# Optimization experiments

Measured on AMD Instinct MI355X. Metric: run time of the kernel, lower is better.

The kernel has to match this reference:

```python
import jax, jax.numpy as jnp
import numpy as np

N_NODES = 131072
N_EDGES = 2097152
N_GRAPHS = 2048
IN_CH, HID, OUT = 12, 64, 4


def gcn_conv(x, W, b, src, dst, n_nodes):
    """PyG GCNConv: out = D^{-1/2} (A + I) D^{-1/2} (x W) + b.
    Degree computed at target nodes including self loops (edge_weight=1)."""
    h = x @ W  # [N, F_out]
    # degree with self loops: in-degree + 1
    deg = jax.ops.segment_sum(jnp.ones((src.shape[0],), x.dtype), dst,
                              num_segments=n_nodes) + 1.0
    dinv = jax.lax.rsqrt(deg)  # [N]
    norm = dinv[src] * dinv[dst]  # [E]
    # scatter-add messages from src to dst
    agg = jax.ops.segment_sum(h[src] * norm[:, None], dst, num_segments=n_nodes)
    # self-loop contribution: norm_ii = dinv[i]^2
    agg = agg + h * (dinv * dinv)[:, None]
    return agg + b


def global_mean_pool(x, batch, n_graphs):
    sums = jax.ops.segment_sum(x, batch, num_segments=n_graphs)
    cnt = jax.ops.segment_sum(jnp.ones((x.shape[0],), x.dtype), batch,
                              num_segments=n_graphs)
    return sums / jnp.maximum(cnt, 1.0)[:, None]


def setup_inputs() -> dict:
    key = jax.random.key(0)
    ks = jax.random.split(key, 9)
    x = jax.random.normal(ks[0], (N_NODES, IN_CH), dtype=jnp.float32)
    edge_index = jax.random.randint(ks[1], (2, N_EDGES), 0, N_NODES, dtype=jnp.int64)
    batch = jnp.sort(jax.random.randint(ks[2], (N_NODES,), 0, N_GRAPHS, dtype=jnp.int64))
    def glorot(k, shape):
        lim = np.sqrt(6.0 / (shape[0] + shape[1]))
        return jax.random.uniform(k, shape, jnp.float32, -lim, lim)
    return {
        "x": x,
        "edge_index": edge_index,
        "batch": batch,
        "W1": glorot(ks[3], (IN_CH, HID)),
        "b1": jnp.zeros((HID,), jnp.float32),
        "W2": glorot(ks[4], (HID, HID)),
        "b2": jnp.zeros((HID,), jnp.float32),
        "Wfc": glorot(ks[5], (HID, OUT)),
        "bfc": jnp.zeros((OUT,), jnp.float32),
    }


def reference(x, edge_index, batch, W1, b1, W2, b2, Wfc, bfc):
    src, dst = edge_index[0], edge_index[1]
    h = jax.nn.relu(gcn_conv(x, W1, b1, src, dst, N_NODES))
    h = jax.nn.relu(gcn_conv(h, W2, b2, src, dst, N_NODES))
    g = global_mean_pool(h, batch, N_GRAPHS)  # [n_graphs, HID]
    return jax.nn.sigmoid(g @ Wfc + bfc)  # [n_graphs, OUT]
```

## Files before the change

### kernel.cpp

```cpp
#include <hip/hip_runtime.h>
#include <hip/hip_bf16.h>


#define N_NODES 131072
#define N_EDGES 2097152
#define N_GRAPHS 2048
#define IN_CH 12
#define HID 64
#define OUT_CH 4
#define NBUCK 512
#define CHUNK 8192
#define STRIDE 4608
#define CSR_STRIDE 5120
#define CAP 5120

typedef float f32x2 __attribute__((ext_vector_type(2)));

__device__ __forceinline__ unsigned short f2bf(float f) {
    unsigned u = __float_as_uint(f);
    return (unsigned short)((u + 0x7fffu + ((u >> 16) & 1u)) >> 16);
}
__device__ __forceinline__ unsigned pack2bf(float lo, float hi) {
    return (unsigned)f2bf(lo) | ((unsigned)f2bf(hi) << 16);
}
__device__ __forceinline__ float bflo(unsigned v) { return __uint_as_float(v << 16); }
__device__ __forceinline__ float bfhi(unsigned v) { return __uint_as_float(v & 0xFFFF0000u); }

__global__ __launch_bounds__(1024, 4)
void bucket_kernel(const int* __restrict__ src, const int* __restrict__ dst,
                   int* __restrict__ bucket_count, int* __restrict__ staged) {
    __shared__ int hist[NBUCK];
    __shared__ int lscan[NBUCK];
    __shared__ int gbase[NBUCK];
    __shared__ int cursor[NBUCK];
    __shared__ int sorted[CHUNK];
    int tid = threadIdx.x;
    int base = blockIdx.x * CHUNK;
    if (tid < NBUCK) { hist[tid] = 0; cursor[tid] = 0; }
    __syncthreads();
    int d8[8], s8[8];
#pragma unroll
    for (int k = 0; k < 8; k++) {
        int i = base + k * 1024 + tid;
        d8[k] = dst[i];
        s8[k] = src[i];
        atomicAdd(&hist[d8[k] >> 8], 1);
    }
    __syncthreads();
    if (tid < NBUCK) lscan[tid] = hist[tid];
    __syncthreads();
    for (int off = 1; off < NBUCK; off <<= 1) {
        int u = (tid < NBUCK && tid >= off) ? lscan[tid - off] : 0;
        __syncthreads();
        if (tid < NBUCK) lscan[tid] += u;
        __syncthreads();
    }
    if (tid < NBUCK) gbase[tid] = atomicAdd(&bucket_count[tid], hist[tid]);
    __syncthreads();
#pragma unroll
    for (int k = 0; k < 8; k++) {
        int b = d8[k] >> 8;
        int start = lscan[b] - hist[b];
        int p = start + atomicAdd(&cursor[b], 1);
        sorted[p] = ((d8[k] & 255) << 17) | s8[k];
    }
    __syncthreads();
    int wid = tid >> 6, lane = tid & 63;
    int g16 = lane >> 4, k16 = lane & 15;
    for (int b0 = wid * 4; b0 < NBUCK; b0 += 64) {
        int b = b0 + g16;
        int cb = hist[b];
        int lbase = lscan[b] - cb;
        int gb = b * STRIDE + gbase[b];
        for (int k = k16; k < cb; k += 16) staged[gb + k] = sorted[lbase + k];
    }
}

__global__ void build_kernel(const int* __restrict__ bucket_count, const int* __restrict__ staged,
                             int2* __restrict__ rowbounds, float* __restrict__ dinv,
                             int* __restrict__ csr, const float* __restrict__ x,
                             unsigned short* __restrict__ xb) {
    __shared__ int sl[STRIDE];
    __shared__ int image[CAP];
    __shared__ int cnt[256];
    __shared__ int scn[256];
    __shared__ int loff[256];
    __shared__ int cursor[256];
    __shared__ int totalS;
    int b = blockIdx.x;
    int tid = threadIdx.x;
    int count = bucket_count[b];
    const int* st = staged + b * STRIDE;
    cnt[tid] = 0;
    cursor[tid] = 0;
    for (int i = tid; i < count; i += 256) sl[i] = st[i];
    __syncthreads();
    for (int i = tid; i < count; i += 256) atomicAdd(&cnt[(sl[i] >> 17) & 255], 1);
    __syncthreads();
    int deg = cnt[tid];
    int degp = (deg + 3) & ~3;
    scn[tid] = degp;
    __syncthreads();
    for (int off = 1; off < 256; off <<= 1) {
        int u = (tid >= off) ? scn[tid - off] : 0;
        __syncthreads();
        scn[tid] += u;
        __syncthreads();
    }
    int lo = scn[tid] - degp;
    loff[tid] = lo;
    int nbase = (b << 8) + tid;
    int gb = b * CSR_STRIDE;
    rowbounds[nbase] = make_int2(gb + lo, gb + lo + degp);
    float dv = rsqrtf((float)deg + 1.0f);
    dinv[nbase] = dv;
    if (tid == 255) totalS = lo + degp;
    {
        const float* xp = x + nbase * IN_CH;
        unsigned o[8];
#pragma unroll
        for (int k = 0; k < 6; k++) o[k] = pack2bf(dv * xp[2 * k], dv * xp[2 * k + 1]);
        o[6] = 0; o[7] = 0;
        uint4* dstp = (uint4*)(xb + nbase * 16);
        dstp[0] = make_uint4(o[0], o[1], o[2], o[3]);
        dstp[1] = make_uint4(o[4], o[5], o[6], o[7]);
    }
    if (b == 0 && tid < 2)
        ((uint4*)(xb + (size_t)N_NODES * 16))[tid] = make_uint4(0, 0, 0, 0);
    __syncthreads();
    for (int i = tid; i < count; i += 256) {
        int rec = sl[i];
        int s = rec & 0x1FFFF;
        int dq = (rec >> 17) & 255;
        int p = loff[dq] + atomicAdd(&cursor[dq], 1);
        int val = s << 6;
        if (p < CAP) image[p] = val;
        else csr[gb + p] = val;
    }
    __syncthreads();
    int padval = N_NODES << 6;
    for (int p = loff[tid] + deg; p < loff[tid] + degp; p++) {
        if (p < CAP) image[p] = padval;
        else csr[gb + p] = padval;
    }
    __syncthreads();
    int lim = totalS < CAP ? totalS : CAP;
    int* dstp = csr + gb;
    for (int i = tid; i < lim; i += 256) dstp[i] = image[i];
}

__global__ __launch_bounds__(256, 6)
void w1w2_kernel(const int2* __restrict__ rowbounds, const int* __restrict__ csr,
                 const float* __restrict__ dinv, const unsigned short* __restrict__ xb,
                 const float* __restrict__ W1, const float* __restrict__ b1,
                 const float* __restrict__ W2, unsigned int* __restrict__ hout) {
    __shared__ float sW1[IN_CH * HID];
    __shared__ float sA[64 * 17];
    __shared__ float sh1t[HID * 65];
    int tid = threadIdx.x;
    for (int i = tid; i < IN_CH * HID; i += 256) sW1[i] = W1[i];
    int node0 = blockIdx.x * 64;
    {
        int nl = tid >> 2;
        int node = node0 + nl;
        int p = tid & 1, qoff = 8 * p;
        int2 rb = rowbounds[node];
        float dn = dinv[node];
        uint4 su = make_uint4(0, 0, 0, 0);
        if (!(tid & 2)) su = *(const uint4*)(xb + node * 16 + qoff);
        int len = rb.y - rb.x;
        int hlen = (len >> 3) << 2;
        int beg = (tid & 2) ? rb.x + hlen : rb.x;
        int end = (tid & 2) ? rb.y : rb.x + hlen;
        f32x2 a0[4] = {{0, 0}, {0, 0}, {0, 0}, {0, 0}};
        f32x2 a1[4] = {{0, 0}, {0, 0}, {0, 0}, {0, 0}};
        f32x2 a2[4] = {{0, 0}, {0, 0}, {0, 0}, {0, 0}};
        f32x2 a3[4] = {{0, 0}, {0, 0}, {0, 0}, {0, 0}};
        for (int j = beg; j < end; j += 4) {
            int4 e = *(const int4*)(csr + j);
            uint4 u0 = *(const uint4*)(xb + (e.x >> 2) + qoff);
            uint4 u1 = *(const uint4*)(xb + (e.y >> 2) + qoff);
            uint4 u2 = *(const uint4*)(xb + (e.z >> 2) + qoff);
            uint4 u3 = *(const uint4*)(xb + (e.w >> 2) + qoff);
            a0[0] += (f32x2){bflo(u0.x), bfhi(u0.x)};
            a0[1] += (f32x2){bflo(u0.y), bfhi(u0.y)};
            a0[2] += (f32x2){bflo(u0.z), bfhi(u0.z)};
            a0[3] += (f32x2){bflo(u0.w), bfhi(u0.w)};
            a1[0] += (f32x2){bflo(u1.x), bfhi(u1.x)};
            a1[1] += (f32x2){bflo(u1.y), bfhi(u1.y)};
            a1[2] += (f32x2){bflo(u1.z), bfhi(u1.z)};
            a1[3] += (f32x2){bflo(u1.w), bfhi(u1.w)};
            a2[0] += (f32x2){bflo(u2.x), bfhi(u2.x)};
            a2[1] += (f32x2){bflo(u2.y), bfhi(u2.y)};
            a2[2] += (f32x2){bflo(u2.z), bfhi(u2.z)};
            a2[3] += (f32x2){bflo(u2.w), bfhi(u2.w)};
            a3[0] += (f32x2){bflo(u3.x), bfhi(u3.x)};
            a3[1] += (f32x2){bflo(u3.y), bfhi(u3.y)};
            a3[2] += (f32x2){bflo(u3.z), bfhi(u3.z)};
            a3[3] += (f32x2){bflo(u3.w), bfhi(u3.w)};
        }
        f32x2 s0 = (a0[0] + a1[0]) + (a2[0] + a3[0]);
        f32x2 s1 = (a0[1] + a1[1]) + (a2[1] + a3[1]);
        f32x2 s2 = (a0[2] + a1[2]) + (a2[2] + a3[2]);
        f32x2 s3 = (a0[3] + a1[3]) + (a2[3] + a3[3]);
        s0[0] += __shfl_xor(s0[0], 2); s0[1] += __shfl_xor(s0[1], 2);
        s1[0] += __shfl_xor(s1[0], 2); s1[1] += __shfl_xor(s1[1], 2);
        s2[0] += __shfl_xor(s2[0], 2); s2[1] += __shfl_xor(s2[1], 2);
        s3[0] += __shfl_xor(s3[0], 2); s3[1] += __shfl_xor(s3[1], 2);
        if (!(tid & 2)) {
            s0 += (f32x2){bflo(su.x), bfhi(su.x)};
            s1 += (f32x2){bflo(su.y), bfhi(su.y)};
            s2 += (f32x2){bflo(su.z), bfhi(su.z)};
            s3 += (f32x2){bflo(su.w), bfhi(su.w)};
            float* dp = &sA[nl * 17 + qoff];
            dp[0] = dn * s0[0]; dp[1] = dn * s0[1];
            dp[2] = dn * s1[0]; dp[3] = dn * s1[1];
            dp[4] = dn * s2[0]; dp[5] = dn * s2[1];
            dp[6] = dn * s3[0]; dp[7] = dn * s3[1];
        }
    }
    __syncthreads();
    int w = tid >> 6, c = tid & 63;
    float bc = b1[c];
#pragma unroll
    for (int it = 0; it < 4; it++) {
        int n0 = w * 16 + it * 4;
        float a0 = bc, a1 = bc, a2 = bc, a3 = bc;
#pragma unroll
        for (int k = 0; k < IN_CH; k++) {
            float wv = sW1[k * HID + c];
            a0 += sA[(n0 + 0) * 17 + k] * wv;
            a1 += sA[(n0 + 1) * 17 + k] * wv;
            a2 += sA[(n0 + 2) * 17 + k] * wv;
            a3 += sA[(n0 + 3) * 17 + k] * wv;
        }
        float4 o = make_float4(fmaxf(a0, 0.0f), fmaxf(a1, 0.0f),
                               fmaxf(a2, 0.0f), fmaxf(a3, 0.0f));
        *(float4*)&sh1t[c * 65 + n0] = o;
    }
    __syncthreads();
    int nq = tid >> 4, c4 = (tid & 15) * 4;
    float4 a0 = {0, 0, 0, 0}, a1 = {0, 0, 0, 0}, a2 = {0, 0, 0, 0}, a3 = {0, 0, 0, 0};
#pragma unroll 4
    for (int k = 0; k < HID; k++) {
        float4 wv = *(const float4*)&W2[k * HID + c4];
        float4 hv = *(const float4*)&sh1t[k * 65 + nq * 4];
        a0.x += hv.x * wv.x; a0.y += hv.x * wv.y; a0.z += hv.x * wv.z; a0.w += hv.x * wv.w;
        a1.x += hv.y * wv.x; a1.y += hv.y * wv.y; a1.z += hv.y * wv.z; a1.w += hv.y * wv.w;
        a2.x += hv.z * wv.x; a2.y += hv.z * wv.y; a2.z += hv.z * wv.z; a2.w += hv.z * wv.w;
        a3.x += hv.w * wv.x; a3.y += hv.w * wv.y; a3.z += hv.w * wv.z; a3.w += hv.w * wv.w;
    }
    int nb = node0 + nq * 4;
    float dv0 = dinv[nb + 0], dv1 = dinv[nb + 1], dv2 = dinv[nb + 2], dv3 = dinv[nb + 3];
    unsigned int p0 = (unsigned int)__builtin_amdgcn_cvt_pk_fp8_f32(dv0 * a0.x, dv0 * a0.y, 0, false);
    p0 = (unsigned int)__builtin_amdgcn_cvt_pk_fp8_f32(dv0 * a0.z, dv0 * a0.w, (int)p0, true);
    unsigned int p1 = (unsigned int)__builtin_amdgcn_cvt_pk_fp8_f32(dv1 * a1.x, dv1 * a1.y, 0, false);
    p1 = (unsigned int)__builtin_amdgcn_cvt_pk_fp8_f32(dv1 * a1.z, dv1 * a1.w, (int)p1, true);
    unsigned int p2 = (unsigned int)__builtin_amdgcn_cvt_pk_fp8_f32(dv2 * a2.x, dv2 * a2.y, 0, false);
    p2 = (unsigned int)__builtin_amdgcn_cvt_pk_fp8_f32(dv2 * a2.z, dv2 * a2.w, (int)p2, true);
    unsigned int p3 = (unsigned int)__builtin_amdgcn_cvt_pk_fp8_f32(dv3 * a3.x, dv3 * a3.y, 0, false);
    p3 = (unsigned int)__builtin_amdgcn_cvt_pk_fp8_f32(dv3 * a3.z, dv3 * a3.w, (int)p3, true);
    int cl = c4 >> 2;
    hout[(nb + 0) * 16 + cl] = p0;
    hout[(nb + 1) * 16 + cl] = p1;
    hout[(nb + 2) * 16 + cl] = p2;
    hout[(nb + 3) * 16 + cl] = p3;
    if (blockIdx.x == 0 && tid < 16)
        hout[(size_t)N_NODES * 16 + tid] = 0;
}

__device__ __forceinline__ void add_fp8q(f32x2* a, uint4 u) {
    a[0] += __builtin_amdgcn_cvt_pk_f32_fp8((int)u.x, false);
    a[1] += __builtin_amdgcn_cvt_pk_f32_fp8((int)u.x, true);
    a[2] += __builtin_amdgcn_cvt_pk_f32_fp8((int)u.y, false);
    a[3] += __builtin_amdgcn_cvt_pk_f32_fp8((int)u.y, true);
    a[4] += __builtin_amdgcn_cvt_pk_f32_fp8((int)u.z, false);
    a[5] += __builtin_amdgcn_cvt_pk_f32_fp8((int)u.z, true);
    a[6] += __builtin_amdgcn_cvt_pk_f32_fp8((int)u.w, false);
    a[7] += __builtin_amdgcn_cvt_pk_f32_fp8((int)u.w, true);
}

__device__ __forceinline__ void agg_body16(int beg, int end, const int* __restrict__ csr,
                                           const unsigned char* __restrict__ h,
                                           int qoff, float* r) {
    f32x2 a0[8] = {{0, 0}, {0, 0}, {0, 0}, {0, 0}, {0, 0}, {0, 0}, {0, 0}, {0, 0}};
    f32x2 a1[8] = {{0, 0}, {0, 0}, {0, 0}, {0, 0}, {0, 0}, {0, 0}, {0, 0}, {0, 0}};
    int j = beg;
    for (; j + 8 <= end; j += 8) {
        int4 ea = *(const int4*)(csr + j);
        int4 eb = *(const int4*)(csr + j + 4);
        uint4 u0 = *(const uint4*)(h + ea.x + qoff);
        uint4 u1 = *(const uint4*)(h + ea.y + qoff);
        uint4 u2 = *(const uint4*)(h + ea.z + qoff);
        uint4 u3 = *(const uint4*)(h + ea.w + qoff);
        uint4 u4 = *(const uint4*)(h + eb.x + qoff);
        uint4 u5 = *(const uint4*)(h + eb.y + qoff);
        uint4 u6 = *(const uint4*)(h + eb.z + qoff);
        uint4 u7 = *(const uint4*)(h + eb.w + qoff);
        add_fp8q(a0, u0); add_fp8q(a1, u1); add_fp8q(a0, u2); add_fp8q(a1, u3);
        add_fp8q(a0, u4); add_fp8q(a1, u5); add_fp8q(a0, u6); add_fp8q(a1, u7);
    }
    if (j < end) {
        int4 ea = *(const int4*)(csr + j);
        uint4 u0 = *(const uint4*)(h + ea.x + qoff);
        uint4 u1 = *(const uint4*)(h + ea.y + qoff);
        uint4 u2 = *(const uint4*)(h + ea.z + qoff);
        uint4 u3 = *(const uint4*)(h + ea.w + qoff);
        add_fp8q(a0, u0); add_fp8q(a1, u1); add_fp8q(a0, u2); add_fp8q(a1, u3);
    }
#pragma unroll
    for (int k = 0; k < 8; k++) {
        f32x2 s = a0[k] + a1[k];
        r[2 * k] = s[0];
        r[2 * k + 1] = s[1];
    }
}

__global__ void agg_pool_kernel(const int2* __restrict__ rowbounds, const int* __restrict__ csr,
                                const float* __restrict__ dinv,
                                const unsigned char* __restrict__ h,
                                const float* __restrict__ b, const int* __restrict__ batch,
                                float* __restrict__ pool, float* __restrict__ gcnt) {
    __shared__ float red[64][HID + 4];
    __shared__ int gids[64];
    int tid = threadIdx.x;
    int w = tid >> 6, lane = tid & 63, sub = lane >> 2, q = lane & 3;
    int qoff = 16 * q;
    int node = (blockIdx.x * 4 + w) * 16 + sub;
    int2 rb = rowbounds[node];
    float dn = dinv[node];
    float r[16];
    agg_body16(rb.x, rb.y, csr, h, qoff, r);
    uint4 su = *(const uint4*)(h + node * HID + qoff);
    f32x2 s[8];
    s[0] = __builtin_amdgcn_cvt_pk_f32_fp8((int)su.x, false);
    s[1] = __builtin_amdgcn_cvt_pk_f32_fp8((int)su.x, true);
    s[2] = __builtin_amdgcn_cvt_pk_f32_fp8((int)su.y, false);
    s[3] = __builtin_amdgcn_cvt_pk_f32_fp8((int)su.y, true);
    s[4] = __builtin_amdgcn_cvt_pk_f32_fp8((int)su.z, false);
    s[5] = __builtin_amdgcn_cvt_pk_f32_fp8((int)su.z, true);
    s[6] = __builtin_amdgcn_cvt_pk_f32_fp8((int)su.w, false);
    s[7] = __builtin_amdgcn_cvt_pk_f32_fp8((int)su.w, true);
    int nl = w * 16 + sub;
    float* rp = &red[nl][qoff];
#pragma unroll
    for (int k = 0; k < 4; k++) {
        float4 bv = *(const float4*)&b[qoff + 4 * k];
        rp[4 * k + 0] = fmaxf(dn * (r[4 * k + 0] + s[2 * k][0]) + bv.x, 0.0f);
        rp[4 * k + 1] = fmaxf(dn * (r[4 * k + 1] + s[2 * k][1]) + bv.y, 0.0f);
        rp[4 * k + 2] = fmaxf(dn * (r[4 * k + 2] + s[2 * k + 1][0]) + bv.z, 0.0f);
        rp[4 * k + 3] = fmaxf(dn * (r[4 * k + 3] + s[2 * k + 1][1]) + bv.w, 0.0f);
    }
    if (q == 0) gids[nl] = batch[node];
    __syncthreads();
    if (tid < 64) {
        int c = tid;
        float acc = 0.0f;
        int cur = gids[0], cnt = 0;
        for (int n = 0; n < 64; n++) {
            int g = gids[n];
            if (g != cur) {
                atomicAdd(&pool[cur * HID + c], acc);
                if (c == 0) atomicAdd(&gcnt[cur], (float)cnt);
                acc = 0.0f; cnt = 0; cur = g;
            }
            acc += red[n][c];
            cnt++;
        }
        atomicAdd(&pool[cur * HID + c], acc);
        if (c == 0) atomicAdd(&gcnt[cur], (float)cnt);
    }
}

__global__ void final_kernel(const float* __restrict__ pool, const float* __restrict__ gcnt,
                             const float* __restrict__ Wfc, const float* __restrict__ bfc,
                             float* __restrict__ out) {
    int idx = blockIdx.x * 256 + threadIdx.x;
    if (idx >= N_GRAPHS * OUT_CH) return;
    int g = idx >> 2, o = idx & 3;
    float inv = 1.0f / fmaxf(gcnt[g], 1.0f);
    float acc = bfc[o];
#pragma unroll
    for (int k = 0; k < HID; k++) acc += pool[g * HID + k] * inv * Wfc[k * OUT_CH + o];
    out[idx] = 1.0f / (1.0f + expf(-acc));
}

extern "C" void kernel_launch(void* const* d_in, const int* in_sizes, int n_in,
                              void* d_out, int out_size, void* d_ws, size_t ws_size,
                              hipStream_t stream) {
    const float* x   = (const float*)d_in[0];
    const int* eidx  = (const int*)d_in[1];
    const int* batch = (const int*)d_in[2];
    const float* W1  = (const float*)d_in[3];
    const float* b1  = (const float*)d_in[4];
    const float* W2  = (const float*)d_in[5];
    const float* b2  = (const float*)d_in[6];
    const float* Wfc = (const float*)d_in[7];
    const float* bfc = (const float*)d_in[8];
    float* out = (float*)d_out;

    const int* src = eidx;
    const int* dst = eidx + N_EDGES;

    unsigned char* hB = (unsigned char*)d_ws;
    int*   csr    = (int*)(hB + (size_t)(N_NODES + 1) * HID);
    int*   staged = csr + (size_t)NBUCK * CSR_STRIDE;
    float* dinv   = (float*)(staged + (size_t)NBUCK * STRIDE);
    int2*  rowbounds = (int2*)(dinv + N_NODES);
    int*   bucket_count = (int*)(rowbounds + N_NODES);
    float* pool   = (float*)(bucket_count + NBUCK);
    float* gcnt   = pool + N_GRAPHS * HID;
    unsigned short* xb = (unsigned short*)(gcnt + N_GRAPHS);

    hipMemsetAsync(bucket_count, 0,
                   (size_t)(NBUCK + N_GRAPHS * HID + N_GRAPHS) * 4, stream);

    bucket_kernel<<<N_EDGES / CHUNK, 1024, 0, stream>>>(src, dst, bucket_count, staged);
    build_kernel<<<NBUCK, 256, 0, stream>>>(bucket_count, staged, rowbounds, dinv, csr, x, xb);

    w1w2_kernel<<<N_NODES / 64, 256, 0, stream>>>(rowbounds, csr, dinv, xb, W1, b1, W2,
                                                  (unsigned int*)hB);

    agg_pool_kernel<<<N_NODES / 64, 256, 0, stream>>>(rowbounds, csr, dinv, hB, b2, batch,
                                                      pool, gcnt);

    final_kernel<<<(N_GRAPHS * OUT_CH + 255) / 256, 256, 0, stream>>>(pool, gcnt, Wfc, bfc, out);
}
```

Baseline: 180.8 us.

## Pack bf16 node features to 24-byte rows and unroll first-layer gather

Stores the scaled bf16 input features as 12 values (24 bytes) per node instead of a padded 32-byte row, so each gathered neighbor row in the first-layer aggregation moves less data. The gather loop is unrolled to eight edges per iteration with a remainder step, W1 is held in registers instead of shared memory, and the launch bound is raised to allow more resident blocks. In the pooling kernel, the self-feature and batch-id loads are hoisted ahead of the neighbor aggregation to overlap their latency. Risks include unaligned 12-byte loads and a changed index decode (3*(e>>4)) that must match the CSR encoding of s<<6.

Result: no change. 182.3 us (+0.8%).

```diff
diff --git a/kernel.cpp b/kernel.cpp
--- a/kernel.cpp
+++ b/kernel.cpp
@@ -117,16 +117,16 @@
     if (tid == 255) totalS = lo + degp;
     {
         const float* xp = x + nbase * IN_CH;
-        unsigned o[8];
+        unsigned o[6];
 #pragma unroll
         for (int k = 0; k < 6; k++) o[k] = pack2bf(dv * xp[2 * k], dv * xp[2 * k + 1]);
-        o[6] = 0; o[7] = 0;
-        uint4* dstp = (uint4*)(xb + nbase * 16);
-        dstp[0] = make_uint4(o[0], o[1], o[2], o[3]);
-        dstp[1] = make_uint4(o[4], o[5], o[6], o[7]);
-    }
-    if (b == 0 && tid < 2)
-        ((uint4*)(xb + (size_t)N_NODES * 16))[tid] = make_uint4(0, 0, 0, 0);
+        uint2* dstp = (uint2*)(xb + nbase * 12);
+        dstp[0] = make_uint2(o[0], o[1]);
+        dstp[1] = make_uint2(o[2], o[3]);
+        dstp[2] = make_uint2(o[4], o[5]);
+    }
+    if (b == 0 && tid < 3)
+        ((uint2*)(xb + (size_t)N_NODES * 12))[tid] = make_uint2(0, 0);
     __syncthreads();
     for (int i = tid; i < count; i += 256) {
         int rec = sl[i];
@@ -149,90 +149,93 @@
     for (int i = tid; i < lim; i += 256) dstp[i] = image[i];
 }
 
-__global__ __launch_bounds__(256, 6)
+__device__ __forceinline__ void acc3(f32x2* a, uint3 u) {
+    a[0] += (f32x2){bflo(u.x), bfhi(u.x)};
+    a[1] += (f32x2){bflo(u.y), bfhi(u.y)};
+    a[2] += (f32x2){bflo(u.z), bfhi(u.z)};
+}
+
+__global__ __launch_bounds__(256, 8)
 void w1w2_kernel(const int2* __restrict__ rowbounds, const int* __restrict__ csr,
                  const float* __restrict__ dinv, const unsigned short* __restrict__ xb,
                  const float* __restrict__ W1, const float* __restrict__ b1,
                  const float* __restrict__ W2, unsigned int* __restrict__ hout) {
-    __shared__ float sW1[IN_CH * HID];
-    __shared__ float sA[64 * 17];
+    __shared__ float sA[64 * 13];
     __shared__ float sh1t[HID * 65];
     int tid = threadIdx.x;
-    for (int i = tid; i < IN_CH * HID; i += 256) sW1[i] = W1[i];
     int node0 = blockIdx.x * 64;
     {
         int nl = tid >> 2;
         int node = node0 + nl;
-        int p = tid & 1, qoff = 8 * p;
+        int p = tid & 1, soff = 6 * p;
         int2 rb = rowbounds[node];
         float dn = dinv[node];
-        uint4 su = make_uint4(0, 0, 0, 0);
-        if (!(tid & 2)) su = *(const uint4*)(xb + node * 16 + qoff);
+        uint3 su = {0, 0, 0};
+        if (!(tid & 2)) su = *(const uint3*)(xb + node * 12 + soff);
         int len = rb.y - rb.x;
         int hlen = (len >> 3) << 2;
         int beg = (tid & 2) ? rb.x + hlen : rb.x;
         int end = (tid & 2) ? rb.y : rb.x + hlen;
-        f32x2 a0[4] = {{0, 0}, {0, 0}, {0, 0}, {0, 0}};
-        f32x2 a1[4] = {{0, 0}, {0, 0}, {0, 0}, {0, 0}};
-        f32x2 a2[4] = {{0, 0}, {0, 0}, {0, 0}, {0, 0}};
-        f32x2 a3[4] = {{0, 0}, {0, 0}, {0, 0}, {0, 0}};
-        for (int j = beg; j < end; j += 4) {
-            int4 e = *(const int4*)(csr + j);
-            uint4 u0 = *(const uint4*)(xb + (e.x >> 2) + qoff);
-            uint4 u1 = *(const uint4*)(xb + (e.y >> 2) + qoff);
-            uint4 u2 = *(const uint4*)(xb + (e.z >> 2) + qoff);
-            uint4 u3 = *(const uint4*)(xb + (e.w >> 2) + qoff);
-            a0[0] += (f32x2){bflo(u0.x), bfhi(u0.x)};
-            a0[1] += (f32x2){bflo(u0.y), bfhi(u0.y)};
-            a0[2] += (f32x2){bflo(u0.z), bfhi(u0.z)};
-            a0[3] += (f32x2){bflo(u0.w), bfhi(u0.w)};
-            a1[0] += (f32x2){bflo(u1.x), bfhi(u1.x)};
-            a1[1] += (f32x2){bflo(u1.y), bfhi(u1.y)};
-            a1[2] += (f32x2){bflo(u1.z), bfhi(u1.z)};
-            a1[3] += (f32x2){bflo(u1.w), bfhi(u1.w)};
-            a2[0] += (f32x2){bflo(u2.x), bfhi(u2.x)};
-            a2[1] += (f32x2){bflo(u2.y), bfhi(u2.y)};
-            a2[2] += (f32x2){bflo(u2.z), bfhi(u2.z)};
-            a2[3] += (f32x2){bflo(u2.w), bfhi(u2.w)};
-            a3[0] += (f32x2){bflo(u3.x), bfhi(u3.x)};
-            a3[1] += (f32x2){bflo(u3.y), bfhi(u3.y)};
-            a3[2] += (f32x2){bflo(u3.z), bfhi(u3.z)};
-            a3[3] += (f32x2){bflo(u3.w), bfhi(u3.w)};
+        f32x2 a0[3] = {{0, 0}, {0, 0}, {0, 0}};
+        f32x2 a1[3] = {{0, 0}, {0, 0}, {0, 0}};
+        f32x2 a2[3] = {{0, 0}, {0, 0}, {0, 0}};
+        f32x2 a3[3] = {{0, 0}, {0, 0}, {0, 0}};
+        int j = beg;
+        for (; j + 8 <= end; j += 8) {
+            int4 ea = *(const int4*)(csr + j);
+            int4 eb = *(const int4*)(csr + j + 4);
+            uint3 u0 = *(const uint3*)(xb + 3 * (ea.x >> 4) + soff);
+            uint3 u1 = *(const uint3*)(xb + 3 * (ea.y >> 4) + soff);
+            uint3 u2 = *(const uint3*)(xb + 3 * (ea.z >> 4) + soff);
+            uint3 u3 = *(const uint3*)(xb + 3 * (ea.w >> 4) + soff);
+            uint3 u4 = *(const uint3*)(xb + 3 * (eb.x >> 4) + soff);
+            uint3 u5 = *(const uint3*)(xb + 3 * (eb.y >> 4) + soff);
+            uint3 u6 = *(const uint3*)(xb + 3 * (eb.z >> 4) + soff);
+            uint3 u7 = *(const uint3*)(xb + 3 * (eb.w >> 4) + soff);
+            acc3(a0, u0); acc3(a1, u1); acc3(a2, u2); acc3(a3, u3);
+            acc3(a0, u4); acc3(a1, u5); acc3(a2, u6); acc3(a3, u7);
+        }
+        if (j < end) {
+            int4 ea = *(const int4*)(csr + j);
+            uint3 u0 = *(const uint3*)(xb + 3 * (ea.x >> 4) + soff);
+            uint3 u1 = *(const uint3*)(xb + 3 * (ea.y >> 4) + soff);
+            uint3 u2 = *(const uint3*)(xb + 3 * (ea.z >> 4) + soff);
+            uint3 u3 = *(const uint3*)(xb + 3 * (ea.w >> 4) + soff);
+            acc3(a0, u0); acc3(a1, u1); acc3(a2, u2); acc3(a3, u3);
         }
         f32x2 s0 = (a0[0] + a1[0]) + (a2[0] + a3[0]);
         f32x2 s1 = (a0[1] + a1[1]) + (a2[1] + a3[1]);
         f32x2 s2 = (a0[2] + a1[2]) + (a2[2] + a3[2]);
-        f32x2 s3 = (a0[3] + a1[3]) + (a2[3] + a3[3]);
         s0[0] += __shfl_xor(s0[0], 2); s0[1] += __shfl_xor(s0[1], 2);
         s1[0] += __shfl_xor(s1[0], 2); s1[1] += __shfl_xor(s1[1], 2);
         s2[0] += __shfl_xor(s2[0], 2); s2[1] += __shfl_xor(s2[1], 2);
-        s3[0] += __shfl_xor(s3[0], 2); s3[1] += __shfl_xor(s3[1], 2);
         if (!(tid & 2)) {
             s0 += (f32x2){bflo(su.x), bfhi(su.x)};
             s1 += (f32x2){bflo(su.y), bfhi(su.y)};
             s2 += (f32x2){bflo(su.z), bfhi(su.z)};
-            s3 += (f32x2){bflo(su.w), bfhi(su.w)};
-            float* dp = &sA[nl * 17 + qoff];
+            float* dp = &sA[nl * 13 + soff];
             dp[0] = dn * s0[0]; dp[1] = dn * s0[1];
             dp[2] = dn * s1[0]; dp[3] = dn * s1[1];
             dp[4] = dn * s2[0]; dp[5] = dn * s2[1];
-            dp[6] = dn * s3[0]; dp[7] = dn * s3[1];
         }
     }
     __syncthreads();
     int w = tid >> 6, c = tid & 63;
     float bc = b1[c];
+    float wk[IN_CH];
+#pragma unroll
+    for (int k = 0; k < IN_CH; k++) wk[k] = W1[k * HID + c];
 #pragma unroll
     for (int it = 0; it < 4; it++) {
         int n0 = w * 16 + it * 4;
         float a0 = bc, a1 = bc, a2 = bc, a3 = bc;
 #pragma unroll
         for (int k = 0; k < IN_CH; k++) {
-            float wv = sW1[k * HID + c];
-            a0 += sA[(n0 + 0) * 17 + k] * wv;
-            a1 += sA[(n0 + 1) * 17 + k] * wv;
-            a2 += sA[(n0 + 2) * 17 + k] * wv;
-            a3 += sA[(n0 + 3) * 17 + k] * wv;
+            float wv = wk[k];
+            a0 += sA[(n0 + 0) * 13 + k] * wv;
+            a1 += sA[(n0 + 1) * 13 + k] * wv;
+            a2 += sA[(n0 + 2) * 13 + k] * wv;
+            a3 += sA[(n0 + 3) * 13 + k] * wv;
         }
         float4 o = make_float4(fmaxf(a0, 0.0f), fmaxf(a1, 0.0f),
                                fmaxf(a2, 0.0f), fmaxf(a3, 0.0f));
@@ -329,9 +332,10 @@
     int node = (blockIdx.x * 4 + w) * 16 + sub;
     int2 rb = rowbounds[node];
     float dn = dinv[node];
+    uint4 su = *(const uint4*)(h + node * HID + qoff);
+    int gid = batch[node];
     float r[16];
     agg_body16(rb.x, rb.y, csr, h, qoff, r);
-    uint4 su = *(const uint4*)(h + node * HID + qoff);
     f32x2 s[8];
     s[0] = __builtin_amdgcn_cvt_pk_f32_fp8((int)su.x, false);
     s[1] = __builtin_amdgcn_cvt_pk_f32_fp8((int)su.x, true);
@@ -351,7 +355,7 @@
         rp[4 * k + 2] = fmaxf(dn * (r[4 * k + 2] + s[2 * k + 1][0]) + bv.z, 0.0f);
         rp[4 * k + 3] = fmaxf(dn * (r[4 * k + 3] + s[2 * k + 1][1]) + bv.w, 0.0f);
     }
-    if (q == 0) gids[nl] = batch[node];
+    if (q == 0) gids[nl] = gid;
     __syncthreads();
     if (tid < 64) {
         int c = tid;
```
